# Kernel tuning notes

Measured on AMD Instinct MI355X. Metric: run time of the kernel, lower is better.

The kernel has to match this reference:

```python
import jax, jax.numpy as jnp
import numpy as np

ALL_PERMS = jnp.array([[0, 1, 2], [0, 2, 1], [1, 0, 2], [1, 2, 0], [2, 0, 1], [2, 1, 0]], dtype=jnp.int32)
ENRICH_CLIP = 100.0
B, D, H = 16384, 512, 512
P_IN = D + 6 + 3   # seq_embed + pres_state(6) + round_onehot(3)
F_IN = D + 12 + 3  # seq_embed + full_state(12) + round_onehot(3)


def _gelu(x):
    return jax.nn.gelu(x, approximate=False)  # keras 'gelu' is erf-based


def _mlp3(x, w1, b1, w2, b2, w3, b3):
    h = _gelu(x @ w1 + b1)
    h = _gelu(h @ w2 + b2)
    return h @ w3 + b3


def setup_inputs() -> dict:
    key = jax.random.key(0)
    ks = jax.random.split(key, 12)
    s = 0.02
    return {
        'seq_embed': jax.random.normal(ks[0], (B, D), jnp.float32),
        'freq': jax.random.normal(ks[1], (B, 3), jnp.float32),
        'pres': (jax.random.uniform(ks[2], (B, 3)) < 0.5).astype(jnp.float32),
        'enrich': jax.random.normal(ks[3], (B, 3), jnp.float32),
        'pw1': jax.random.normal(ks[4], (P_IN, H), jnp.float32) * s, 'pb1': jnp.zeros((H,), jnp.float32),
        'pw2': jax.random.normal(ks[5], (H, H // 2), jnp.float32) * s, 'pb2': jnp.zeros((H // 2,), jnp.float32),
        'pw3': jax.random.normal(ks[6], (H // 2, 1), jnp.float32) * s, 'pb3': jnp.zeros((1,), jnp.float32),
        'fw1': jax.random.normal(ks[7], (F_IN, H), jnp.float32) * s, 'fb1': jnp.zeros((H,), jnp.float32),
        'fw2': jax.random.normal(ks[8], (H, H), jnp.float32) * s, 'fb2': jnp.zeros((H,), jnp.float32),
        'fw3': jax.random.normal(ks[9], (H, 2), jnp.float32) * s, 'fb3': jnp.zeros((2,), jnp.float32),
        'perm_idx': jax.random.randint(ks[10], (B,), 0, 6, dtype=jnp.int32),
        'round_mask': jax.random.randint(ks[11], (B, 3), 0, 2, dtype=jnp.int32),
    }


def _decode(seq_embed, freq, pres, enrich, mask_f, perms,
            pw1, pb1, pw2, pb2, pw3, pb3, fw1, fb1, fw2, fb2, fw3, fb3):
    Bn = seq_embed.shape[0]
    dt = seq_embed.dtype
    ones = jnp.ones((Bn,), dt)
    pres_state = jnp.zeros((Bn, 3, 2), dt)  # [R, (pres, decoded_flag)]
    full_state = jnp.zeros((Bn, 3, 4), dt)  # [R, (freq, pres, enrich, decoded_flag)]
    d_f = jnp.zeros((Bn, 3), dt)
    d_p = jnp.zeros((Bn, 3), dt)
    d_e = jnp.zeros((Bn, 3), dt)
    lf = lp = le = nm = jnp.float32(0.0)
    for step in range(3):
        ridx = perms[:, step]                               # [B]
        r_oh = jax.nn.one_hot(ridx, 3, dtype=dt)            # [B,3]
        take = lambda a: jnp.take_along_axis(a, ridx[:, None], axis=1)[:, 0]
        gt_f, gt_p, gt_e, m = take(freq), take(pres), take(enrich), take(mask_f)
        pres_inp = jnp.concatenate([seq_embed, pres_state.reshape(Bn, 6), r_oh], axis=1)
        pp_logit = _mlp3(pres_inp, pw1, pb1, pw2, pb2, pw3, pb3)[:, 0]
        fe_inp = jnp.concatenate([seq_embed, full_state.reshape(Bn, 12), r_oh], axis=1)
        fe_pred = _mlp3(fe_inp, fw1, fb1, fw2, fb2, fw3, fb3)
        pf, pe = fe_pred[:, 0], fe_pred[:, 1]
        lf = lf + jnp.sum(jnp.square(pf - gt_f) * m)
        bce = jnp.maximum(pp_logit, 0.0) - pp_logit * gt_p + jnp.log1p(jnp.exp(-jnp.abs(pp_logit)))
        lp = lp + jnp.sum(bce * m)
        le = le + jnp.sum(jnp.square(pe - gt_e) * m)
        nm = nm + jnp.sum(m)
        msk = m > 0.5
        act_f = jnp.where(msk, jnp.clip(pf, -10.0, 10.0), gt_f)
        act_p = jnp.where(msk, jax.nn.sigmoid(pp_logit), gt_p)
        act_e = jnp.where(msk, jnp.clip(pe, -ENRICH_CLIP, ENRICH_CLIP), gt_e)
        sel = r_oh[:, :, None]  # equal-mask scatter into the ridx-th slot
        pres_state = pres_state * (1.0 - sel) + jnp.stack([act_p, ones], axis=1)[:, None, :] * sel
        full_state = full_state * (1.0 - sel) + jnp.stack([act_f, act_p, act_e, ones], axis=1)[:, None, :] * sel
        d_f = d_f * (1.0 - r_oh) + act_f[:, None] * r_oh
        d_p = d_p * (1.0 - r_oh) + act_p[:, None] * r_oh
        d_e = d_e * (1.0 - r_oh) + act_e[:, None] * r_oh
    nm = nm + 1e-08
    return lf / nm, lp / nm, le / nm, d_f, d_p, d_e


def reference(seq_embed, freq, pres, enrich,
              pw1, pb1, pw2, pb2, pw3, pb3,
              fw1, fb1, fw2, fb2, fw3, fb3,
              perm_idx, round_mask):
    perms = ALL_PERMS[perm_idx]                      # [B,3] random round orders
    mask_f = round_mask.astype(seq_embed.dtype)      # [B,3] 0/1 mask
    lf, lp, le, d_f, d_p, d_e = _decode(seq_embed, freq, pres, enrich, mask_f, perms,
                                        pw1, pb1, pw2, pb2, pw3, pb3,
                                        fw1, fb1, fw2, fb2, fw3, fb3)
    # flat layout: [loss_freq, loss_pres, loss_enrich, dec_freq(B*3), dec_pres(B*3), dec_enrich(B*3)]
    return jnp.concatenate([jnp.stack([lf, lp, le]), d_f.ravel(), d_p.ravel(), d_e.ravel()])
```

## Files before the change

### kernel.cpp

```cpp
#include <hip/hip_runtime.h>
#include <hip/hip_bf16.h>
#include <math.h>

#define BATCH 16384

typedef unsigned short u16;
typedef short bf16x8 __attribute__((ext_vector_type(8)));
typedef float f32x4 __attribute__((ext_vector_type(4)));
typedef u16 u16x8 __attribute__((ext_vector_type(8)));
typedef u16 u16x4 __attribute__((ext_vector_type(4)));

__constant__ int PERMS_C[6][3] = {{0,1,2},{0,2,1},{1,0,2},{1,2,0},{2,0,1},{2,1,0}};

__device__ inline float bf2f(u16 u) {
    unsigned int x = ((unsigned int)u) << 16;
    float f; __builtin_memcpy(&f, &x, 4); return f;
}
__device__ inline u16 f2bf(float f) {
    __hip_bfloat16 h = __float2bfloat16(f);
    u16 u; __builtin_memcpy(&u, &h, 2); return u;
}
__device__ inline float gelu_exact(float x) {
    return 0.5f * x * (1.0f + erff(x * 0.70710678118654752f));
}

__global__ __launch_bounds__(256) void prep_kernel(
    const float* __restrict__ seq,
    const float* __restrict__ pw1, const float* __restrict__ pw2,
    const float* __restrict__ fw1, const float* __restrict__ fw2,
    const float* __restrict__ pb1, const float* __restrict__ pb2,
    const float* __restrict__ fb1, const float* __restrict__ fb2,
    u16* __restrict__ sb, u16* __restrict__ W1T, u16* __restrict__ W2T,
    float* __restrict__ bias1, float* __restrict__ bias2,
    float* __restrict__ states)
{
    const int N0 = BATCH * 512;
    const int N1 = 1024 * 512;
    const int N2 = 768 * 512;
    const int N3 = 1024;
    const int N4 = 768;
    const int N5 = BATCH * 18;
    int i = blockIdx.x * 256 + threadIdx.x;
    if (i < N0) { sb[i] = f2bf(seq[i]); return; }
    i -= N0;
    if (i < N1) {
        int n = i >> 9, k = i & 511;
        float v = (n < 512) ? pw1[(size_t)k * 512 + n] : fw1[(size_t)k * 512 + (n - 512)];
        W1T[i] = f2bf(v); return;
    }
    i -= N1;
    if (i < N2) {
        int n = i >> 9, k = i & 511;
        float v = (n < 256) ? pw2[(size_t)k * 256 + n] : fw2[(size_t)k * 512 + (n - 256)];
        W2T[i] = f2bf(v); return;
    }
    i -= N2;
    if (i < N3) { bias1[i] = (i < 512) ? pb1[i] : fb1[i - 512]; return; }
    i -= N3;
    if (i < N4) { bias2[i] = (i < 256) ? pb2[i] : fb2[i - 256]; return; }
    i -= N4;
    if (i < N5) { states[i] = 0.0f; return; }
}

#define LDP 72

__global__ __launch_bounds__(256) void gemm_bf16(
    const u16* __restrict__ A0, const u16* __restrict__ A1, int lda,
    const u16* __restrict__ Bt, const float* __restrict__ bias,
    u16* __restrict__ C, int M, int N, int K, int n_split, int apply_gelu)
{
    __shared__ __align__(16) u16 As[128 * LDP];
    __shared__ __align__(16) u16 Bs[128 * LDP];

    const int bm = blockIdx.x * 128;
    const int bn = blockIdx.y * 128;
    const u16* __restrict__ A = (bn < n_split) ? A0 : A1;

    const int tid = threadIdx.x;
    const int wave = tid >> 6;
    const int lane = tid & 63;
    const int wr = wave >> 1;
    const int wc = wave & 1;

    f32x4 acc[4][4];
#pragma unroll
    for (int i = 0; i < 4; ++i)
#pragma unroll
        for (int j = 0; j < 4; ++j) acc[i][j] = (f32x4){0.f, 0.f, 0.f, 0.f};

    for (int k0 = 0; k0 < K; k0 += 64) {
#pragma unroll
        for (int c = 0; c < 4; ++c) {
            int chunk = tid + c * 256;
            int row = chunk >> 3;
            int col8 = (chunk & 7) << 3;
            uint4 va = *reinterpret_cast<const uint4*>(&A[(size_t)(bm + row) * lda + k0 + col8]);
            *reinterpret_cast<uint4*>(&As[row * LDP + col8]) = va;
            uint4 vb = *reinterpret_cast<const uint4*>(&Bt[(size_t)(bn + row) * K + k0 + col8]);
            *reinterpret_cast<uint4*>(&Bs[row * LDP + col8]) = vb;
        }
        __syncthreads();

#pragma unroll
        for (int ks = 0; ks < 64; ks += 32) {
            int kk = ks + (lane >> 4) * 8;
            bf16x8 af[4], bfr[4];
#pragma unroll
            for (int i = 0; i < 4; ++i)
                af[i] = *reinterpret_cast<const bf16x8*>(&As[(wr * 64 + i * 16 + (lane & 15)) * LDP + kk]);
#pragma unroll
            for (int j = 0; j < 4; ++j)
                bfr[j] = *reinterpret_cast<const bf16x8*>(&Bs[(wc * 64 + j * 16 + (lane & 15)) * LDP + kk]);
#pragma unroll
            for (int i = 0; i < 4; ++i)
#pragma unroll
                for (int j = 0; j < 4; ++j)
                    acc[i][j] = __builtin_amdgcn_mfma_f32_16x16x32_bf16(af[i], bfr[j], acc[i][j], 0, 0, 0);
        }
        __syncthreads();
    }

    const int r4 = (lane >> 4) * 4;
    const int cn = lane & 15;
#pragma unroll
    for (int i = 0; i < 4; ++i) {
#pragma unroll
        for (int j = 0; j < 4; ++j) {
            int gcol = bn + wc * 64 + j * 16 + cn;
            float bsv = bias[gcol];
#pragma unroll
            for (int r = 0; r < 4; ++r) {
                int grow = bm + wr * 64 + i * 16 + r4 + r;
                float v = acc[i][j][r] + bsv;
                if (apply_gelu) v = gelu_exact(v);
                C[(size_t)grow * N + gcol] = f2bf(v);
            }
        }
    }
}

template<int NSTATE>
__global__ __launch_bounds__(256) void step_h1_t(
    const u16* __restrict__ Z, const float* __restrict__ wsrc,
    const float* __restrict__ state, const int* __restrict__ perm_idx, int step,
    u16* __restrict__ H1, int colBase)
{
    constexpr int NR = NSTATE + 3;
    const int tid = threadIdx.x;
    const int c64 = tid & 63;
    const int ws = tid >> 6;
    const int col0 = c64 * 8;

    float w[NR][8];
#pragma unroll
    for (int t = 0; t < NR; ++t) {
        float4 a = *reinterpret_cast<const float4*>(&wsrc[(size_t)t * 512 + col0]);
        float4 b = *reinterpret_cast<const float4*>(&wsrc[(size_t)t * 512 + col0 + 4]);
        w[t][0] = a.x; w[t][1] = a.y; w[t][2] = a.z; w[t][3] = a.w;
        w[t][4] = b.x; w[t][5] = b.y; w[t][6] = b.z; w[t][7] = b.w;
    }

    int row = blockIdx.x * 16 + ws;
#pragma unroll 2
    for (int i = 0; i < 4; ++i, row += 4) {
        const int ridx = PERMS_C[perm_idx[row]][step];
        float s0[NSTATE];
        if constexpr (NSTATE == 6) {
            float2 a = *reinterpret_cast<const float2*>(&state[row * 6]);
            float2 b = *reinterpret_cast<const float2*>(&state[row * 6 + 2]);
            float2 c = *reinterpret_cast<const float2*>(&state[row * 6 + 4]);
            s0[0] = a.x; s0[1] = a.y; s0[2] = b.x; s0[3] = b.y; s0[4] = c.x; s0[5] = c.y;
        } else {
            float4 a = *reinterpret_cast<const float4*>(&state[row * 12]);
            float4 b = *reinterpret_cast<const float4*>(&state[row * 12 + 4]);
            float4 c = *reinterpret_cast<const float4*>(&state[row * 12 + 8]);
            s0[0] = a.x; s0[1] = a.y; s0[2]  = a.z; s0[3]  = a.w;
            s0[4] = b.x; s0[5] = b.y; s0[6]  = b.z; s0[7]  = b.w;
            s0[8] = c.x; s0[9] = c.y; s0[10] = c.z; s0[11] = c.w;
        }
        u16x8 z = *reinterpret_cast<const u16x8*>(&Z[(size_t)row * 1024 + colBase + col0]);
        u16x8 o;
#pragma unroll
        for (int e = 0; e < 8; ++e) {
            float d = (ridx == 0) ? w[NSTATE][e]
                    : ((ridx == 1) ? w[NSTATE + 1][e] : w[NSTATE + 2][e]);
#pragma unroll
            for (int t = 0; t < NSTATE; ++t) d += s0[t] * w[t][e];
            o[e] = f2bf(gelu_exact(bf2f(z[e]) + d));
        }
        *reinterpret_cast<u16x8*>(&H1[(size_t)row * 1024 + colBase + col0]) = o;
    }
}

__global__ __launch_bounds__(256) void step_head(
    const u16* __restrict__ H2,
    const float* __restrict__ pw3, const float* __restrict__ pb3,
    const float* __restrict__ fw3, const float* __restrict__ fb3,
    const float* __restrict__ freq, const float* __restrict__ presv,
    const float* __restrict__ enrich,
    const int* __restrict__ round_mask, const int* __restrict__ perm_idx, int step,
    float* __restrict__ pres_state, float* __restrict__ full_state,
    float* __restrict__ part, float* __restrict__ out)
{
    const int wid = threadIdx.x >> 6;
    const int lane = threadIdx.x & 63;
    const int row0 = blockIdx.x * 16;

    __shared__ float lg[16][4];

    float4 wp = *reinterpret_cast<const float4*>(&pw3[lane * 4]);
    float4 wa = *reinterpret_cast<const float4*>(&fw3[lane * 16]);
    float4 wb = *reinterpret_cast<const float4*>(&fw3[lane * 16 + 4]);
    float4 wc = *reinterpret_cast<const float4*>(&fw3[lane * 16 + 8]);
    float4 wd = *reinterpret_cast<const float4*>(&fw3[lane * 16 + 12]);

#pragma unroll
    for (int i = 0; i < 4; ++i) {
        const int r = wid * 4 + i;
        const int b = row0 + r;
        const u16* h2 = &H2[(size_t)b * 768];

        u16x4 hp = *reinterpret_cast<const u16x4*>(&h2[lane * 4]);
        float sp = bf2f(hp[0]) * wp.x + bf2f(hp[1]) * wp.y
                 + bf2f(hp[2]) * wp.z + bf2f(hp[3]) * wp.w;

        u16x8 hf = *reinterpret_cast<const u16x8*>(&h2[256 + lane * 8]);
        float h0 = bf2f(hf[0]), h1 = bf2f(hf[1]), h2v = bf2f(hf[2]), h3 = bf2f(hf[3]);
        float h4 = bf2f(hf[4]), h5 = bf2f(hf[5]), h6v = bf2f(hf[6]), h7 = bf2f(hf[7]);
        float sf = h0 * wa.x + h1 * wa.z + h2v * wb.x + h3 * wb.z
                 + h4 * wc.x + h5 * wc.z + h6v * wd.x + h7 * wd.z;
        float se = h0 * wa.y + h1 * wa.w + h2v * wb.y + h3 * wb.w
                 + h4 * wc.y + h5 * wc.w + h6v * wd.y + h7 * wd.w;

        for (int off = 32; off > 0; off >>= 1) {
            sp += __shfl_down(sp, off);
            sf += __shfl_down(sf, off);
            se += __shfl_down(se, off);
        }
        if (lane == 0) { lg[r][0] = sp; lg[r][1] = sf; lg[r][2] = se; }
    }
    __syncthreads();

    float lf = 0.f, bce = 0.f, le = 0.f, mm = 0.f;
    if (wid == 0) {
        if (lane < 16) {
            const int b = row0 + lane;
            float logit = lg[lane][0] + pb3[0];
            float pf    = lg[lane][1] + fb3[0];
            float pe    = lg[lane][2] + fb3[1];
            int ridx = PERMS_C[perm_idx[b]][step];
            float gt_f = freq[b * 3 + ridx];
            float gt_p = presv[b * 3 + ridx];
            float gt_e = enrich[b * 3 + ridx];
            float m = (float)round_mask[b * 3 + ridx];
            lf  = (pf - gt_f) * (pf - gt_f) * m;
            bce = (fmaxf(logit, 0.f) - logit * gt_p + log1pf(expf(-fabsf(logit)))) * m;
            le  = (pe - gt_e) * (pe - gt_e) * m;
            mm  = m;
            bool msk = m > 0.5f;
            float act_f = msk ? fminf(fmaxf(pf, -10.f), 10.f) : gt_f;
            float act_p = msk ? 1.f / (1.f + expf(-logit)) : gt_p;
            float act_e = msk ? fminf(fmaxf(pe, -100.f), 100.f) : gt_e;
            pres_state[b * 6 + ridx * 2 + 0] = act_p;
            pres_state[b * 6 + ridx * 2 + 1] = 1.f;
            full_state[b * 12 + ridx * 4 + 0] = act_f;
            full_state[b * 12 + ridx * 4 + 1] = act_p;
            full_state[b * 12 + ridx * 4 + 2] = act_e;
            full_state[b * 12 + ridx * 4 + 3] = 1.f;
            out[3 + b * 3 + ridx] = act_f;
            out[3 + 3 * BATCH + b * 3 + ridx] = act_p;
            out[3 + 6 * BATCH + b * 3 + ridx] = act_e;
        }
        for (int off = 8; off > 0; off >>= 1) {
            lf  += __shfl_down(lf, off);
            bce += __shfl_down(bce, off);
            le  += __shfl_down(le, off);
            mm  += __shfl_down(mm, off);
        }
        if (lane == 0) {
            float4 v; v.x = lf; v.y = bce; v.z = le; v.w = mm;
            *reinterpret_cast<float4*>(&part[blockIdx.x * 4]) = v;
        }
    }
}

#define HEAD_BLOCKS (BATCH / 16)

__global__ __launch_bounds__(256) void finalize_kernel(
    const float* __restrict__ part, float* __restrict__ out)
{
    __shared__ float red[4][4];
    const int nslots = 3 * HEAD_BLOCKS;
    float a0 = 0.f, a1 = 0.f, a2 = 0.f, a3 = 0.f;
    for (int j = threadIdx.x; j < nslots; j += 256) {
        float4 v = *reinterpret_cast<const float4*>(&part[j * 4]);
        a0 += v.x; a1 += v.y; a2 += v.z; a3 += v.w;
    }
    for (int off = 32; off > 0; off >>= 1) {
        a0 += __shfl_down(a0, off);
        a1 += __shfl_down(a1, off);
        a2 += __shfl_down(a2, off);
        a3 += __shfl_down(a3, off);
    }
    const int wid = threadIdx.x >> 6, lane = threadIdx.x & 63;
    if (lane == 0) { red[wid][0] = a0; red[wid][1] = a1; red[wid][2] = a2; red[wid][3] = a3; }
    __syncthreads();
    if (threadIdx.x == 0) {
        float s0 = 0.f, s1 = 0.f, s2 = 0.f, s3 = 0.f;
#pragma unroll
        for (int w2 = 0; w2 < 4; ++w2) {
            s0 += red[w2][0]; s1 += red[w2][1]; s2 += red[w2][2]; s3 += red[w2][3];
        }
        float nm = s3 + 1e-8f;
        out[0] = s0 / nm;
        out[1] = s1 / nm;
        out[2] = s2 / nm;
    }
}

extern "C" void kernel_launch(void* const* d_in, const int* in_sizes, int n_in,
                              void* d_out, int out_size, void* d_ws, size_t ws_size,
                              hipStream_t stream)
{
    const float* seq       = (const float*)d_in[0];
    const float* freq      = (const float*)d_in[1];
    const float* presv     = (const float*)d_in[2];
    const float* enrich    = (const float*)d_in[3];
    const float* pw1       = (const float*)d_in[4];
    const float* pb1       = (const float*)d_in[5];
    const float* pw2       = (const float*)d_in[6];
    const float* pb2       = (const float*)d_in[7];
    const float* pw3       = (const float*)d_in[8];
    const float* pb3       = (const float*)d_in[9];
    const float* fw1       = (const float*)d_in[10];
    const float* fb1       = (const float*)d_in[11];
    const float* fw2       = (const float*)d_in[12];
    const float* fb2       = (const float*)d_in[13];
    const float* fw3       = (const float*)d_in[14];
    const float* fb3       = (const float*)d_in[15];
    const int*   perm_idx  = (const int*)d_in[16];
    const int*   round_mask= (const int*)d_in[17];
    float* out = (float*)d_out;

    char* w = (char*)d_ws;
    u16* sb  = (u16*)w;  w += (size_t)BATCH * 512 * 2;
    u16* Z   = (u16*)w;  w += (size_t)BATCH * 1024 * 2;
    u16* H1  = (u16*)w;  w += (size_t)BATCH * 1024 * 2;
    u16* H2  = (u16*)w;  w += (size_t)BATCH * 768 * 2;
    u16* W1T = (u16*)w;  w += (size_t)1024 * 512 * 2;
    u16* W2T = (u16*)w;  w += (size_t)768 * 512 * 2;
    float* bias1 = (float*)w; w += 1024 * 4;
    float* bias2 = (float*)w; w += 768 * 4;
    float* states = (float*)w; w += (size_t)BATCH * 18 * 4;
    float* part   = (float*)w;
    float* pres_state = states;
    float* full_state = states + (size_t)BATCH * 6;

    {
        const int total = BATCH * 512 + 1024 * 512 + 768 * 512 + 1024 + 768 + BATCH * 18;
        int grid = (total + 255) / 256;
        prep_kernel<<<grid, 256, 0, stream>>>(seq, pw1, pw2, fw1, fw2, pb1, pb2, fb1, fb2,
                                              sb, W1T, W2T, bias1, bias2, states);
    }

    gemm_bf16<<<dim3(BATCH / 128, 1024 / 128), 256, 0, stream>>>(
        sb, sb, 512, W1T, bias1, Z, BATCH, 1024, 512, 1 << 30, 0);

    for (int s = 0; s < 3; ++s) {
        step_h1_t<6><<<BATCH / 16, 256, 0, stream>>>(
            Z, pw1 + (size_t)512 * 512, pres_state, perm_idx, s, H1, 0);
        step_h1_t<12><<<BATCH / 16, 256, 0, stream>>>(
            Z, fw1 + (size_t)512 * 512, full_state, perm_idx, s, H1, 512);

        gemm_bf16<<<dim3(BATCH / 128, 768 / 128), 256, 0, stream>>>(
            H1, H1 + 512, 1024, W2T, bias2, H2, BATCH, 768, 512, 256, 1);

        step_head<<<HEAD_BLOCKS, 256, 0, stream>>>(
            H2, pw3, pb3, fw3, fb3, freq, presv, enrich,
            round_mask, perm_idx, s, pres_state, full_state,
            part + (size_t)s * HEAD_BLOCKS * 4, out);
    }

    finalize_kernel<<<1, 256, 0, stream>>>(part, out);
}
```

Before: 380.9 us.

## Use direct global-to-LDS loads in GEMM and merge step_h1 kernels

The GEMM tile loads now use the global_load_lds builtin, which writes global data straight into shared memory without staging it through registers. The shared tiles drop their padding (stride 64 instead of 72) to fit the contiguous 64-lane write layout. Dropping the padding may add LDS bank conflicts on the MFMA fragment reads. Separately, the two per-step h1 kernels are merged into one launch with a 2-wide grid to cut launch overhead.

```diff
diff --git a/kernel.cpp b/kernel.cpp
--- a/kernel.cpp
+++ b/kernel.cpp
@@ -22,6 +22,13 @@
 }
 __device__ inline float gelu_exact(float x) {
     return 0.5f * x * (1.0f + erff(x * 0.70710678118654752f));
+}
+
+__device__ inline void gload_lds16(const u16* g, u16* l) {
+    __builtin_amdgcn_global_load_lds(
+        (const __attribute__((address_space(1))) unsigned int*)g,
+        (__attribute__((address_space(3))) unsigned int*)l,
+        16, 0, 0);
 }
 
 __global__ __launch_bounds__(256) void prep_kernel(
@@ -62,25 +69,26 @@
     if (i < N5) { states[i] = 0.0f; return; }
 }
 
-#define LDP 72
-
 __global__ __launch_bounds__(256) void gemm_bf16(
     const u16* __restrict__ A0, const u16* __restrict__ A1, int lda,
     const u16* __restrict__ Bt, const float* __restrict__ bias,
     u16* __restrict__ C, int M, int N, int K, int n_split, int apply_gelu)
 {
-    __shared__ __align__(16) u16 As[128 * LDP];
-    __shared__ __align__(16) u16 Bs[128 * LDP];
+    __shared__ __align__(16) u16 As[128 * 64];
+    __shared__ __align__(16) u16 Bs[128 * 64];
 
     const int bm = blockIdx.x * 128;
     const int bn = blockIdx.y * 128;
     const u16* __restrict__ A = (bn < n_split) ? A0 : A1;
 
     const int tid = threadIdx.x;
-    const int wave = tid >> 6;
+    const int wv = tid >> 6;
     const int lane = tid & 63;
-    const int wr = wave >> 1;
-    const int wc = wave & 1;
+    const int wr = wv >> 1;
+    const int wc = wv & 1;
+
+    const int lrow = lane >> 3;
+    const int lcol = (lane & 7) << 3;
 
     f32x4 acc[4][4];
 #pragma unroll
@@ -90,14 +98,11 @@
 
     for (int k0 = 0; k0 < K; k0 += 64) {
 #pragma unroll
-        for (int c = 0; c < 4; ++c) {
-            int chunk = tid + c * 256;
-            int row = chunk >> 3;
-            int col8 = (chunk & 7) << 3;
-            uint4 va = *reinterpret_cast<const uint4*>(&A[(size_t)(bm + row) * lda + k0 + col8]);
-            *reinterpret_cast<uint4*>(&As[row * LDP + col8]) = va;
-            uint4 vb = *reinterpret_cast<const uint4*>(&Bt[(size_t)(bn + row) * K + k0 + col8]);
-            *reinterpret_cast<uint4*>(&Bs[row * LDP + col8]) = vb;
+        for (int q = 0; q < 4; ++q) {
+            const int c = wv * 4 + q;
+            const int row = c * 8 + lrow;
+            gload_lds16(&A[(size_t)(bm + row) * lda + k0 + lcol], &As[c * 512]);
+            gload_lds16(&Bt[(size_t)(bn + row) * K + k0 + lcol], &Bs[c * 512]);
         }
         __syncthreads();
 
@@ -107,10 +112,10 @@
             bf16x8 af[4], bfr[4];
 #pragma unroll
             for (int i = 0; i < 4; ++i)
-                af[i] = *reinterpret_cast<const bf16x8*>(&As[(wr * 64 + i * 16 + (lane & 15)) * LDP + kk]);
+                af[i] = *reinterpret_cast<const bf16x8*>(&As[(wr * 64 + i * 16 + (lane & 15)) * 64 + kk]);
 #pragma unroll
             for (int j = 0; j < 4; ++j)
-                bfr[j] = *reinterpret_cast<const bf16x8*>(&Bs[(wc * 64 + j * 16 + (lane & 15)) * LDP + kk]);
+                bfr[j] = *reinterpret_cast<const bf16x8*>(&Bs[(wc * 64 + j * 16 + (lane & 15)) * 64 + kk]);
 #pragma unroll
             for (int i = 0; i < 4; ++i)
 #pragma unroll
@@ -140,7 +145,7 @@
 }
 
 template<int NSTATE>
-__global__ __launch_bounds__(256) void step_h1_t(
+__device__ inline void step_h1_body(
     const u16* __restrict__ Z, const float* __restrict__ wsrc,
     const float* __restrict__ state, const int* __restrict__ perm_idx, int step,
     u16* __restrict__ H1, int colBase)
@@ -190,6 +195,18 @@
         }
         *reinterpret_cast<u16x8*>(&H1[(size_t)row * 1024 + colBase + col0]) = o;
     }
+}
+
+__global__ __launch_bounds__(256) void step_h1_both(
+    const u16* __restrict__ Z,
+    const float* __restrict__ pw1s, const float* __restrict__ fw1s,
+    const float* __restrict__ pres_state, const float* __restrict__ full_state,
+    const int* __restrict__ perm_idx, int step, u16* __restrict__ H1)
+{
+    if (blockIdx.y == 0)
+        step_h1_body<6>(Z, pw1s, pres_state, perm_idx, step, H1, 0);
+    else
+        step_h1_body<12>(Z, fw1s, full_state, perm_idx, step, H1, 512);
 }
 
 __global__ __launch_bounds__(256) void step_head(
@@ -367,10 +384,9 @@
         sb, sb, 512, W1T, bias1, Z, BATCH, 1024, 512, 1 << 30, 0);
 
     for (int s = 0; s < 3; ++s) {
-        step_h1_t<6><<<BATCH / 16, 256, 0, stream>>>(
-            Z, pw1 + (size_t)512 * 512, pres_state, perm_idx, s, H1, 0);
-        step_h1_t<12><<<BATCH / 16, 256, 0, stream>>>(
-            Z, fw1 + (size_t)512 * 512, full_state, perm_idx, s, H1, 512);
+        step_h1_both<<<dim3(BATCH / 16, 2), 256, 0, stream>>>(
+            Z, pw1 + (size_t)512 * 512, fw1 + (size_t)512 * 512,
+            pres_state, full_state, perm_idx, s, H1);
 
         gemm_bf16<<<dim3(BATCH / 128, 768 / 128), 256, 0, stream>>>(
             H1, H1 + 512, 1024, W2T, bias2, H2, BATCH, 768, 512, 256, 1);
```

Result: slower. 392.6 us (+3.1%).
